# Performance work log

Hardware: AMD Instinct MI355X
Metric: run time of the kernel (lower is better)

Reference implementation:

```python
import jax, jax.numpy as jnp
import numpy as np

B, H, V, MAX_MSG_LEN = 8192, 512, 512, 16


def _uniform(key, shape, scale):
    return jax.random.uniform(key, shape, jnp.float32, -scale, scale)


def setup_inputs() -> dict:
    key = jax.random.key(0)
    ks = jax.random.split(key, 9)
    s = 1.0 / np.sqrt(H)  # torch LSTMCell/Linear default init scale
    return {
        "encoder_hidden": jax.random.normal(ks[0], (B, H), jnp.float32),
        "encoder_cell": jax.random.normal(ks[1], (B, H), jnp.float32),
        "W_ih": _uniform(ks[2], (4 * H, V), s),   # LSTMCell input weights (i,f,g,o)
        "W_hh": _uniform(ks[3], (4 * H, H), s),   # LSTMCell hidden weights
        "b_ih": _uniform(ks[4], (4 * H,), s),
        "b_hh": _uniform(ks[5], (4 * H,), s),
        "W_out": _uniform(ks[6], (V, H), s),      # nn.Linear(hidden, io_size)
        "b_out": _uniform(ks[7], (V,), s),
        "init_input": jnp.zeros((1, V), jnp.float32),  # nn.Parameter zeros
    }


def reference(encoder_hidden, encoder_cell, W_ih, W_hh, b_ih, b_hh, W_out, b_out, init_input):
    batch = encoder_hidden.shape[0]
    x0 = jnp.broadcast_to(init_input, (batch, init_input.shape[1]))

    def step(carry, _):
        x, h, c, m, lp = carry
        # torch LSTMCell: gates ordered (i, f, g, o)
        gates = x @ W_ih.T + b_ih + h @ W_hh.T + b_hh
        i, f, g, o = jnp.split(gates, 4, axis=-1)
        c = jax.nn.sigmoid(f) * c + jax.nn.sigmoid(i) * jnp.tanh(g)
        h = jax.nn.sigmoid(o) * jnp.tanh(c)
        probs = jax.nn.softmax(h @ W_out.T + b_out, axis=1)  # [B, V]
        # eval path: one-hot of argmax
        predict = jax.nn.one_hot(jnp.argmax(probs, axis=1), probs.shape[1], dtype=probs.dtype)
        lp = lp + jnp.log((probs * predict).sum(axis=1)) * m
        new_m = m * (1.0 - predict[:, -1])  # last vocab index acts as EOS
        return (predict, h, c, new_m, lp), (predict, m)

    carry0 = (x0, encoder_hidden, encoder_cell,
              jnp.ones((batch,), jnp.float32), jnp.zeros((batch,), jnp.float32))
    (_, _, _, _, log_probs), (message, masks) = jax.lax.scan(step, carry0, None, length=MAX_MSG_LEN)
    # message: [L, B, V]; mask stacked as [L, 1, B] like torch.stack of [1, B] rows
    return message, masks[:, None, :], log_probs
```

## Files before the change

kernel.cpp:

```cpp
#include <hip/hip_runtime.h>
#include <math.h>

#define Bsz 8192
#define Hd  512
#define Vd  512
#define Ld  16
#define G4  2048
#define NSLAB 16

using short8 = __attribute__((ext_vector_type(8))) short;
using f32x4  = __attribute__((ext_vector_type(4))) float;
using int4v  = __attribute__((ext_vector_type(4))) int;

__device__ __forceinline__ float sigm_f(float x){
  return __builtin_amdgcn_rcpf(1.0f + __expf(-x));
}
__device__ __forceinline__ float tanh_f(float x){
  return 1.0f - 2.0f * __builtin_amdgcn_rcpf(1.0f + __expf(2.0f * x));
}

__device__ __forceinline__ unsigned short f2bf(float f){
  unsigned int u = __float_as_uint(f);
  u = (u + 0x7fffu + ((u >> 16) & 1u)) >> 16;
  return (unsigned short)u;
}
__device__ __forceinline__ float bf2f(unsigned short b){
  return __uint_as_float(((unsigned int)b) << 16);
}

__device__ __forceinline__ void i16split(float x, float S, signed char& a, signed char& b){
  int q = (int)rintf(x * S);
  q = min(max(q, -32640), 32639);
  const int ah = (q + 128) >> 8;
  a = (signed char)ah;
  b = (signed char)(q - (ah << 8));
}

__device__ __forceinline__ void gl_lds16(const void* g, void* l){
  __builtin_amdgcn_global_load_lds((const __attribute__((address_space(1))) void*)g,
                                   (__attribute__((address_space(3))) void*)l, 16, 0, 0);
}

#define C1I (65536.0f / (524288.0f * 32767.0f))
#define C2I (  256.0f / (524288.0f * 32767.0f))

__global__ __launch_bounds__(256) void k_transpose(const float* __restrict__ in,
                                                   float* __restrict__ out){
  __shared__ float tile[32][33];
  const int tx = threadIdx.x, ty = threadIdx.y;
  const int v0 = blockIdx.x * 32, n0 = blockIdx.y * 32;
#pragma unroll
  for(int i=0;i<4;i++)
    tile[ty+i*8][tx] = in[(size_t)(n0+ty+i*8)*Vd + v0+tx];
  __syncthreads();
#pragma unroll
  for(int i=0;i<4;i++)
    out[(size_t)(v0+ty+i*8)*G4 + n0+tx] = tile[tx][ty+i*8];
}

__global__ __launch_bounds__(256) void k_split(const float* __restrict__ src,
                                               unsigned short* __restrict__ hi,
                                               unsigned short* __restrict__ lo, int n){
  const int i = blockIdx.x*256 + threadIdx.x;
  if(i < n){
    const float x = src[i];
    const unsigned short h = f2bf(x);
    hi[i] = h;
    lo[i] = f2bf(x - bf2f(h));
  }
}

__global__ __launch_bounds__(256) void k_split_i8(const float* __restrict__ src,
                                                  signed char* __restrict__ pa,
                                                  signed char* __restrict__ pb,
                                                  float S, int n){
  const int i = blockIdx.x*256 + threadIdx.x;
  if(i < n){
    signed char a, b;
    i16split(src[i], S, a, b);
    pa[i] = a; pb[i] = b;
  }
}

__global__ __launch_bounds__(256, 2) void k_lstm_bf16(
    const unsigned short* __restrict__ hh, const unsigned short* __restrict__ hl,
    const float* __restrict__ cin,
    signed char* __restrict__ ha, signed char* __restrict__ hb,
    float* __restrict__ cout,
    const unsigned short* __restrict__ Whh_hi, const unsigned short* __restrict__ Whh_lo,
    const float* __restrict__ bih, const float* __restrict__ bhh)
{
  __shared__ unsigned short lds[2][16384];
  const int tid = threadIdx.x;
  const int wave = tid >> 6, lane = tid & 63;
  const int mb = blockIdx.x * 128;
  const int jb = blockIdx.y * 32;
  const int b_wave = (wave & 1) * 64;
  const int j_wave = (wave >> 1) * 16;
  const int fr = lane & 15, q = lane >> 4;
  const int lr = lane >> 2, jj = lane & 3;

  auto stage = [&](int k0, int bsel){
    unsigned short* Whi = lds[bsel];
    unsigned short* Wlo = lds[bsel] + 4096;
    unsigned short* Hhi = lds[bsel] + 8192;
    unsigned short* Hlo = lds[bsel] + 12288;
#pragma unroll
    for(int p=0;p<2;p++){
      const int s = wave*2 + p;
      const int r = s*16 + lr;
      const int j = jj ^ ((r >> 1) & 3);
      const size_t ka = (size_t)k0 + j*8;
      const size_t wrow = (size_t)((r >> 5)*Hd + jb + (r & 31));
      gl_lds16(Whh_hi + wrow*Hd + ka, &Whi[s*512]);
      gl_lds16(Whh_lo + wrow*Hd + ka, &Wlo[s*512]);
      gl_lds16(hh + (size_t)(mb + r)*Hd + ka, &Hhi[s*512]);
      gl_lds16(hl + (size_t)(mb + r)*Hd + ka, &Hlo[s*512]);
    }
  };

  stage(0, 0);

  const int j0 = jb + j_wave + q*4;
  float bsum[4][4];
#pragma unroll
  for(int g=0;g<4;g++){
    float4 a = *(const float4*)&bih[g*Hd + j0];
    float4 b = *(const float4*)&bhh[g*Hd + j0];
    bsum[g][0]=a.x+b.x; bsum[g][1]=a.y+b.y; bsum[g][2]=a.z+b.z; bsum[g][3]=a.w+b.w;
  }

  f32x4 acc[4][4];
#pragma unroll
  for(int g=0;g<4;g++)
#pragma unroll
    for(int bt=0;bt<4;bt++) acc[g][bt] = (f32x4){0.f,0.f,0.f,0.f};

  for(int kc=0; kc<16; kc++){
    __syncthreads();
    if(kc < 15) stage((kc+1)*32, (kc+1)&1);

    const unsigned short* Whi = lds[kc&1];
    const unsigned short* Wlo = lds[kc&1] + 4096;
    const unsigned short* Hhi = lds[kc&1] + 8192;
    const unsigned short* Hlo = lds[kc&1] + 12288;

    short8 wh[4], wl[4], hf[4], lf[4];
#pragma unroll
    for(int g=0;g<4;g++){
      const int r = g*32 + j_wave + fr;
      const int off = r*32 + ((q ^ ((r >> 1) & 3)) << 3);
      wh[g] = *(const short8*)&Whi[off];
      wl[g] = *(const short8*)&Wlo[off];
    }
#pragma unroll
    for(int bt=0;bt<4;bt++){
      const int r = b_wave + bt*16 + fr;
      const int off = r*32 + ((q ^ ((r >> 1) & 3)) << 3);
      hf[bt] = *(const short8*)&Hhi[off];
      lf[bt] = *(const short8*)&Hlo[off];
    }
#pragma unroll
    for(int g=0;g<4;g++)
#pragma unroll
      for(int bt=0;bt<4;bt++){
        acc[g][bt] = __builtin_amdgcn_mfma_f32_16x16x32_bf16(wh[g], hf[bt], acc[g][bt], 0,0,0);
        acc[g][bt] = __builtin_amdgcn_mfma_f32_16x16x32_bf16(wh[g], lf[bt], acc[g][bt], 0,0,0);
        acc[g][bt] = __builtin_amdgcn_mfma_f32_16x16x32_bf16(wl[g], hf[bt], acc[g][bt], 0,0,0);
      }
  }

#pragma unroll
  for(int bt=0;bt<4;bt++){
    const int b = mb + b_wave + bt*16 + fr;
    const size_t idx = (size_t)b*Hd + j0;
    float gv[4][4];
#pragma unroll
    for(int g=0;g<4;g++)
#pragma unroll
      for(int r=0;r<4;r++) gv[g][r] = acc[g][bt][r] + bsum[g][r];
    float co[4];
    *(float4*)co = *(const float4*)&cin[idx];
    float cn[4];
    signed char a4[4], b4[4];
#pragma unroll
    for(int r=0;r<4;r++){
      const float I = sigm_f(gv[0][r]);
      const float F = sigm_f(gv[1][r]);
      const float G = tanh_f(gv[2][r]);
      const float O = sigm_f(gv[3][r]);
      cn[r] = F*co[r] + I*G;
      const float hn = O*tanh_f(cn[r]);
      i16split(hn, 32767.0f, a4[r], b4[r]);
    }
    *(float4*)&cout[idx] = *(float4*)cn;
    *(char4*)&ha[idx] = *(char4*)a4;
    *(char4*)&hb[idx] = *(char4*)b4;
  }
}

__global__ __launch_bounds__(256, 2) void k_lstm_i8(
    const signed char* __restrict__ hA, const signed char* __restrict__ hB,
    const float* __restrict__ cin,
    signed char* __restrict__ hoA, signed char* __restrict__ hoB,
    float* __restrict__ cout,
    const signed char* __restrict__ WA, const signed char* __restrict__ WB,
    const float* __restrict__ WihT, const float* __restrict__ bih,
    const float* __restrict__ bhh,
    const float* __restrict__ statM, const float* __restrict__ statS,
    const int* __restrict__ statI,
    float* __restrict__ msg, float* __restrict__ masks_out,
    float* __restrict__ lp_out, float* __restrict__ lpbuf,
    float* __restrict__ mbuf, int prev)
{
  __shared__ unsigned char lds[2][32768];
  __shared__ int gIs[128];
  const int tid = threadIdx.x;
  const int wave = tid >> 6, lane = tid & 63;
  const int mb = blockIdx.x * 128;
  const int jb = blockIdx.y * 32;
  const int b_wave = (wave & 1) * 64;
  const int j_wave = (wave >> 1) * 16;
  const int fr = lane & 15, q = lane >> 4;
  const int lr = lane >> 2, jj = lane & 3;

  auto stage = [&](int k0, int bsel){
    unsigned char* Wa = lds[bsel];
    unsigned char* Wb = lds[bsel] + 8192;
    unsigned char* Ha = lds[bsel] + 16384;
    unsigned char* Hb = lds[bsel] + 24576;
#pragma unroll
    for(int p=0;p<2;p++){
      const int s = wave*2 + p;
      const int r = s*16 + lr;
      const int j = jj ^ ((r >> 1) & 3);
      const size_t ka = (size_t)k0 + j*16;
      const size_t wrow = (size_t)((r >> 5)*Hd + jb + (r & 31));
      gl_lds16(WA + wrow*Hd + ka, &Wa[s*1024]);
      gl_lds16(WB + wrow*Hd + ka, &Wb[s*1024]);
      gl_lds16(hA + (size_t)(mb + r)*Hd + ka, &Ha[s*1024]);
      gl_lds16(hB + (size_t)(mb + r)*Hd + ka, &Hb[s*1024]);
    }
  };

  stage(0, 0);

  if(tid < 128){
    const int row = mb + tid;
    float gm = statM[row]; int gi = statI[row];
#pragma unroll
    for(int s=1;s<NSLAB;s++){
      const float m = statM[(size_t)s*Bsz + row];
      if(m > gm){ gm = m; gi = statI[(size_t)s*Bsz + row]; }
    }
    if(blockIdx.y == 0){
      float tot = 0.0f;
#pragma unroll
      for(int s=0;s<NSLAB;s++)
        tot += statS[(size_t)s*Bsz + row] * __expf(statM[(size_t)s*Bsz + row] - gm);
      const float logp = -__logf(tot);
      const float mo  = (prev == 0) ? 1.0f : mbuf[row];
      const float lpo = (prev == 0) ? 0.0f : lpbuf[row];
      const float lpn = lpo + logp * mo;
      masks_out[(size_t)prev * Bsz + row] = mo;
      lp_out[row] = lpn;
      lpbuf[row]  = lpn;
      mbuf[row]   = mo * ((gi == Vd-1) ? 0.0f : 1.0f);
    }
    gIs[tid] = gi;
  }
  __syncthreads();

  {
    const int r  = tid >> 1;
    const int c0 = jb + (tid & 1) * 16;
    const int gi = gIs[r];
    float* mrow = msg + ((size_t)prev * Bsz + mb + r) * Vd;
#pragma unroll
    for(int i=0;i<4;i++){
      const int c = c0 + i*4;
      float4 v;
      v.x = (c   == gi) ? 1.0f : 0.0f;
      v.y = (c+1 == gi) ? 1.0f : 0.0f;
      v.z = (c+2 == gi) ? 1.0f : 0.0f;
      v.w = (c+3 == gi) ? 1.0f : 0.0f;
      *(float4*)&mrow[c] = v;
    }
  }

  int xid[4];
#pragma unroll
  for(int bt=0;bt<4;bt++)
    xid[bt] = gIs[b_wave + bt*16 + fr];

  int4v acc1[4][4], acc2[4][4];
#pragma unroll
  for(int g=0;g<4;g++)
#pragma unroll
    for(int bt=0;bt<4;bt++){
      acc1[g][bt] = (int4v){0,0,0,0};
      acc2[g][bt] = (int4v){0,0,0,0};
    }

  for(int kc=0; kc<8; kc++){
    __syncthreads();
    if(kc < 7) stage((kc+1)*64, (kc+1)&1);

    const unsigned char* Wa = lds[kc&1];
    const unsigned char* Wb = lds[kc&1] + 8192;
    const unsigned char* Ha = lds[kc&1] + 16384;
    const unsigned char* Hb = lds[kc&1] + 24576;

    int4v wa[4], wb[4], hf[4], lf[4];
#pragma unroll
    for(int g=0;g<4;g++){
      const int r = g*32 + j_wave + fr;
      const int off = r*64 + ((q ^ ((r >> 1) & 3)) << 4);
      wa[g] = *(const int4v*)&Wa[off];
      wb[g] = *(const int4v*)&Wb[off];
    }
#pragma unroll
    for(int bt=0;bt<4;bt++){
      const int r = b_wave + bt*16 + fr;
      const int off = r*64 + ((q ^ ((r >> 1) & 3)) << 4);
      hf[bt] = *(const int4v*)&Ha[off];
      lf[bt] = *(const int4v*)&Hb[off];
    }
#pragma unroll
    for(int g=0;g<4;g++)
#pragma unroll
      for(int bt=0;bt<4;bt++){
        acc1[g][bt] = __builtin_amdgcn_mfma_i32_16x16x64_i8(wa[g], hf[bt], acc1[g][bt], 0,0,0);
        acc2[g][bt] = __builtin_amdgcn_mfma_i32_16x16x64_i8(wa[g], lf[bt], acc2[g][bt], 0,0,0);
        acc2[g][bt] = __builtin_amdgcn_mfma_i32_16x16x64_i8(wb[g], hf[bt], acc2[g][bt], 0,0,0);
      }
  }

  const int j0 = jb + j_wave + q*4;
  float bsum[4][4];
#pragma unroll
  for(int g=0;g<4;g++){
    float4 a = *(const float4*)&bih[g*Hd + j0];
    float4 b = *(const float4*)&bhh[g*Hd + j0];
    bsum[g][0]=a.x+b.x; bsum[g][1]=a.y+b.y; bsum[g][2]=a.z+b.z; bsum[g][3]=a.w+b.w;
  }
#pragma unroll
  for(int bt=0;bt<4;bt++){
    const int b = mb + b_wave + bt*16 + fr;
    const size_t idx = (size_t)b*Hd + j0;
    float gv[4][4];
#pragma unroll
    for(int g=0;g<4;g++)
#pragma unroll
      for(int r=0;r<4;r++)
        gv[g][r] = fmaf(C1I, (float)acc1[g][bt][r],
                   fmaf(C2I, (float)acc2[g][bt][r], bsum[g][r]));
    {
      const float* grow = WihT + (size_t)xid[bt]*G4 + j0;
#pragma unroll
      for(int g=0;g<4;g++){
        float4 x = *(const float4*)&grow[g*Hd];
        gv[g][0]+=x.x; gv[g][1]+=x.y; gv[g][2]+=x.z; gv[g][3]+=x.w;
      }
    }
    float co[4];
    *(float4*)co = *(const float4*)&cin[idx];
    float cn[4];
    signed char a4[4], b4[4];
#pragma unroll
    for(int r=0;r<4;r++){
      const float I = sigm_f(gv[0][r]);
      const float F = sigm_f(gv[1][r]);
      const float G = tanh_f(gv[2][r]);
      const float O = sigm_f(gv[3][r]);
      cn[r] = F*co[r] + I*G;
      const float hn = O*tanh_f(cn[r]);
      i16split(hn, 32767.0f, a4[r], b4[r]);
    }
    *(float4*)&cout[idx] = *(float4*)cn;
    *(char4*)&hoA[idx] = *(char4*)a4;
    *(char4*)&hoB[idx] = *(char4*)b4;
  }
}

__global__ __launch_bounds__(256, 2) void k_logits_i8(
    const signed char* __restrict__ hA, const signed char* __restrict__ hB,
    const signed char* __restrict__ WoA, const signed char* __restrict__ WoB,
    const float* __restrict__ bout,
    float* __restrict__ statM, float* __restrict__ statS, int* __restrict__ statI)
{
  __shared__ unsigned char lds[2][24576];
  const int tid = threadIdx.x;
  const int wave = tid >> 6, lane = tid & 63;
  const int mb = blockIdx.x * 128;
  const int vb = blockIdx.y * 64;
  const int m_wave = (wave & 1) * 64;
  const int n_wave = (wave >> 1) * 32;
  const int fr = lane & 15, q = lane >> 4;
  const int lr = lane >> 2, jj = lane & 3;

  auto stage = [&](int k0, int bsel){
    unsigned char* Ha = lds[bsel];
    unsigned char* Hb = lds[bsel] + 8192;
    unsigned char* Wa = lds[bsel] + 16384;
    unsigned char* Wb = lds[bsel] + 20480;
#pragma unroll
    for(int p=0;p<2;p++){
      const int s = wave*2 + p;
      const int r = s*16 + lr;
      const int j = jj ^ ((r >> 1) & 3);
      const size_t ka = (size_t)k0 + j*16;
      gl_lds16(hA + (size_t)(mb + r)*Hd + ka, &Ha[s*1024]);
      gl_lds16(hB + (size_t)(mb + r)*Hd + ka, &Hb[s*1024]);
    }
    {
      const int r = wave*16 + lr;
      const int j = jj ^ ((r >> 1) & 3);
      const size_t ka = (size_t)k0 + j*16;
      gl_lds16(WoA + (size_t)(vb + r)*Hd + ka, &Wa[wave*1024]);
      gl_lds16(WoB + (size_t)(vb + r)*Hd + ka, &Wb[wave*1024]);
    }
  };

  stage(0, 0);

  int4v acc1[2][4], acc2[2][4];
#pragma unroll
  for(int nt=0;nt<2;nt++)
#pragma unroll
    for(int mt=0;mt<4;mt++){
      acc1[nt][mt] = (int4v){0,0,0,0};
      acc2[nt][mt] = (int4v){0,0,0,0};
    }

  for(int kc=0; kc<8; kc++){
    __syncthreads();
    if(kc < 7) stage((kc+1)*64, (kc+1)&1);

    const unsigned char* Ha = lds[kc&1];
    const unsigned char* Hb = lds[kc&1] + 8192;
    const unsigned char* Wa = lds[kc&1] + 16384;
    const unsigned char* Wb = lds[kc&1] + 20480;

    int4v ah[4], al[4], bh[2], bl[2];
#pragma unroll
    for(int mt=0;mt<4;mt++){
      const int r = m_wave + mt*16 + fr;
      const int off = r*64 + ((q ^ ((r >> 1) & 3)) << 4);
      ah[mt] = *(const int4v*)&Ha[off];
      al[mt] = *(const int4v*)&Hb[off];
    }
#pragma unroll
    for(int nt=0;nt<2;nt++){
      const int r = n_wave + nt*16 + fr;
      const int off = r*64 + ((q ^ ((r >> 1) & 3)) << 4);
      bh[nt] = *(const int4v*)&Wa[off];
      bl[nt] = *(const int4v*)&Wb[off];
    }
#pragma unroll
    for(int nt=0;nt<2;nt++)
#pragma unroll
      for(int mt=0;mt<4;mt++){
        acc1[nt][mt] = __builtin_amdgcn_mfma_i32_16x16x64_i8(ah[mt], bh[nt], acc1[nt][mt], 0,0,0);
        acc2[nt][mt] = __builtin_amdgcn_mfma_i32_16x16x64_i8(ah[mt], bl[nt], acc2[nt][mt], 0,0,0);
        acc2[nt][mt] = __builtin_amdgcn_mfma_i32_16x16x64_i8(al[mt], bh[nt], acc2[nt][mt], 0,0,0);
      }
  }

  const int slab = blockIdx.y*2 + (wave >> 1);
  float bo[2];
  int vv[2];
#pragma unroll
  for(int nt=0;nt<2;nt++){
    vv[nt] = vb + n_wave + nt*16 + fr;
    bo[nt] = bout[vv[nt]];
  }
#pragma unroll
  for(int mt=0;mt<4;mt++){
#pragma unroll
    for(int reg=0;reg<4;reg++){
      float lg[2];
#pragma unroll
      for(int nt=0;nt<2;nt++)
        lg[nt] = fmaf(C1I, (float)acc1[nt][mt][reg],
                 fmaf(C2I, (float)acc2[nt][mt][reg], bo[nt]));
      float vmax = lg[0];
      int   imax = vv[0];
      if(lg[1] > vmax || (lg[1] == vmax && vv[1] < imax)){ vmax = lg[1]; imax = vv[1]; }
#pragma unroll
      for(int off=1; off<16; off<<=1){
        const float vo = __shfl_xor(vmax, off);
        const int   io = __shfl_xor(imax, off);
        if(vo > vmax || (vo == vmax && io < imax)){ vmax = vo; imax = io; }
      }
      float s = __expf(lg[0] - vmax) + __expf(lg[1] - vmax);
#pragma unroll
      for(int off=1; off<16; off<<=1) s += __shfl_xor(s, off);
      if(fr == 0){
        const int m = mb + m_wave + mt*16 + q*4 + reg;
        statM[(size_t)slab*Bsz + m] = vmax;
        statS[(size_t)slab*Bsz + m] = s;
        statI[(size_t)slab*Bsz + m] = imax;
      }
    }
  }
}

__global__ __launch_bounds__(256) void k_merge(
    const float* __restrict__ statM, const float* __restrict__ statS,
    const int* __restrict__ statI,
    float* __restrict__ msg, float* __restrict__ masks_out,
    float* __restrict__ lp_out, float* __restrict__ lpbuf,
    float* __restrict__ mbuf, int step)
{
  __shared__ int gI[32];
  const int tid = threadIdx.x;
  const int mb = blockIdx.x * 32;

  if(tid < 32){
    const int row = mb + tid;
    float gm = statM[row]; int gi = statI[row];
#pragma unroll
    for(int s=1;s<NSLAB;s++){
      const float m = statM[(size_t)s*Bsz + row];
      if(m > gm){ gm = m; gi = statI[(size_t)s*Bsz + row]; }
    }
    float tot = 0.0f;
#pragma unroll
    for(int s=0;s<NSLAB;s++)
      tot += statS[(size_t)s*Bsz + row] * __expf(statM[(size_t)s*Bsz + row] - gm);
    const float logp = -__logf(tot);
    const float mo  = mbuf[row];
    const float lpn = lpbuf[row] + logp * mo;
    masks_out[(size_t)step * Bsz + row] = mo;
    lp_out[row] = lpn;
    gI[tid] = gi;
  }
  __syncthreads();

  const int r  = tid >> 3;
  const int c8 = tid & 7;
  const int gi = gI[r];
  float* mrow = msg + ((size_t)step * Bsz + mb + r) * Vd;
#pragma unroll
  for(int i=0;i<16;i++){
    const int c = (i*8 + c8) * 4;
    float4 v;
    v.x = (c   == gi) ? 1.0f : 0.0f;
    v.y = (c+1 == gi) ? 1.0f : 0.0f;
    v.z = (c+2 == gi) ? 1.0f : 0.0f;
    v.w = (c+3 == gi) ? 1.0f : 0.0f;
    *(float4*)&mrow[c] = v;
  }
}

extern "C" void kernel_launch(void* const* d_in, const int* in_sizes, int n_in,
                              void* d_out, int out_size, void* d_ws, size_t ws_size,
                              hipStream_t stream) {
  const float* enc_h = (const float*)d_in[0];
  const float* enc_c = (const float*)d_in[1];
  const float* Wih   = (const float*)d_in[2];
  const float* Whh   = (const float*)d_in[3];
  const float* bih   = (const float*)d_in[4];
  const float* bhh   = (const float*)d_in[5];
  const float* Wout  = (const float*)d_in[6];
  const float* bout  = (const float*)d_in[7];

  float* out_msg   = (float*)d_out;
  float* out_masks = out_msg + (size_t)Ld * Bsz * Vd;
  float* out_lp    = out_masks + (size_t)Ld * Bsz;

  char* ws = (char*)d_ws;
  float* WihT  = (float*)ws;          ws += (size_t)Vd * G4 * 4;
  unsigned short* WhhHi = (unsigned short*)ws; ws += (size_t)G4 * Hd * 2;
  unsigned short* WhhLo = (unsigned short*)ws; ws += (size_t)G4 * Hd * 2;
  unsigned short* encHi = (unsigned short*)ws; ws += (size_t)Bsz * Hd * 2;
  unsigned short* encLo = (unsigned short*)ws; ws += (size_t)Bsz * Hd * 2;
  signed char* WhhA = (signed char*)ws; ws += (size_t)G4 * Hd;
  signed char* WhhB = (signed char*)ws; ws += (size_t)G4 * Hd;
  signed char* WoA  = (signed char*)ws; ws += (size_t)Vd * Hd;
  signed char* WoB  = (signed char*)ws; ws += (size_t)Vd * Hd;
  signed char* ha0  = (signed char*)ws; ws += (size_t)Bsz * Hd;
  signed char* hb0  = (signed char*)ws; ws += (size_t)Bsz * Hd;
  signed char* ha1  = (signed char*)ws; ws += (size_t)Bsz * Hd;
  signed char* hb1  = (signed char*)ws; ws += (size_t)Bsz * Hd;
  float* cbuf   = (float*)ws;  ws += (size_t)Bsz * Hd * 4;
  float* statM  = (float*)ws;  ws += (size_t)NSLAB * Bsz * 4;
  float* statS  = (float*)ws;  ws += (size_t)NSLAB * Bsz * 4;
  int*   statI  = (int*)ws;    ws += (size_t)NSLAB * Bsz * 4;
  float* lpbuf  = (float*)ws;  ws += (size_t)Bsz * 4;
  float* mbuf   = (float*)ws;  ws += (size_t)Bsz * 4;

  k_transpose<<<dim3(Vd/32, G4/32), dim3(32,8), 0, stream>>>(Wih, WihT);
  k_split<<<(G4*Hd+255)/256, 256, 0, stream>>>(Whh, WhhHi, WhhLo, G4*Hd);
  k_split<<<(Bsz*Hd+255)/256, 256, 0, stream>>>(enc_h, encHi, encLo, Bsz*Hd);
  k_split_i8<<<(G4*Hd+255)/256, 256, 0, stream>>>(Whh, WhhA, WhhB, 524288.0f, G4*Hd);
  k_split_i8<<<(Vd*Hd+255)/256, 256, 0, stream>>>(Wout, WoA, WoB, 524288.0f, Vd*Hd);

  for(int t=0; t<Ld; t++){
    signed char* haOut = (t & 1) ? ha1 : ha0;
    signed char* hbOut = (t & 1) ? hb1 : hb0;
    const signed char* haIn = (t & 1) ? ha0 : ha1;
    const signed char* hbIn = (t & 1) ? hb0 : hb1;

    if(t == 0){
      k_lstm_bf16<<<dim3(Bsz/128, Hd/32), 256, 0, stream>>>(
          encHi, encLo, enc_c, haOut, hbOut, cbuf, WhhHi, WhhLo, bih, bhh);
    } else {
      k_lstm_i8<<<dim3(Bsz/128, Hd/32), 256, 0, stream>>>(
          haIn, hbIn, cbuf, haOut, hbOut, cbuf, WhhA, WhhB, WihT, bih, bhh,
          statM, statS, statI, out_msg, out_masks, out_lp, lpbuf, mbuf, t-1);
    }
    k_logits_i8<<<dim3(Bsz/128, Vd/64), 256, 0, stream>>>(
        haOut, hbOut, WoA, WoB, bout, statM, statS, statI);
  }
  k_merge<<<Bsz/32, 256, 0, stream>>>(statM, statS, statI,
                                      out_msg, out_masks, out_lp,
                                      lpbuf, mbuf, Ld-1);
}
```

Measured before the change: 1.205 ms.

## Load MFMA operands directly from global memory, dropping LDS staging in LSTM and logits kernels

Both int8 MFMA GEMM kernels (LSTM gates and output logits) stop staging W and h tiles through double-buffered LDS with global-to-LDS loads and barriers. Each lane now reads its 16-byte fragments straight from global memory using precomputed row offsets, and the k loop is unrolled by 2. This removes the __syncthreads and LDS traffic and frees LDS for occupancy. In exchange, operands shared across waves are fetched repeatedly through L1/L2, there is no explicit prefetch overlap, and per-lane 16-byte accesses spread across 16 rows are poorly coalesced.

```diff
diff --git a/kernel.cpp b/kernel.cpp
--- a/kernel.cpp
+++ b/kernel.cpp
@@ -213,7 +213,6 @@
     float* __restrict__ lp_out, float* __restrict__ lpbuf,
     float* __restrict__ mbuf, int prev)
 {
-  __shared__ unsigned char lds[2][32768];
   __shared__ int gIs[128];
   const int tid = threadIdx.x;
   const int wave = tid >> 6, lane = tid & 63;
@@ -222,28 +221,6 @@
   const int b_wave = (wave & 1) * 64;
   const int j_wave = (wave >> 1) * 16;
   const int fr = lane & 15, q = lane >> 4;
-  const int lr = lane >> 2, jj = lane & 3;
-
-  auto stage = [&](int k0, int bsel){
-    unsigned char* Wa = lds[bsel];
-    unsigned char* Wb = lds[bsel] + 8192;
-    unsigned char* Ha = lds[bsel] + 16384;
-    unsigned char* Hb = lds[bsel] + 24576;
-#pragma unroll
-    for(int p=0;p<2;p++){
-      const int s = wave*2 + p;
-      const int r = s*16 + lr;
-      const int j = jj ^ ((r >> 1) & 3);
-      const size_t ka = (size_t)k0 + j*16;
-      const size_t wrow = (size_t)((r >> 5)*Hd + jb + (r & 31));
-      gl_lds16(WA + wrow*Hd + ka, &Wa[s*1024]);
-      gl_lds16(WB + wrow*Hd + ka, &Wb[s*1024]);
-      gl_lds16(hA + (size_t)(mb + r)*Hd + ka, &Ha[s*1024]);
-      gl_lds16(hB + (size_t)(mb + r)*Hd + ka, &Hb[s*1024]);
-    }
-  };
-
-  stage(0, 0);
 
   if(tid < 128){
     const int row = mb + tid;
@@ -293,6 +270,14 @@
   for(int bt=0;bt<4;bt++)
     xid[bt] = gIs[b_wave + bt*16 + fr];
 
+  size_t wro[4], hro[4];
+#pragma unroll
+  for(int g=0;g<4;g++)
+    wro[g] = (size_t)(g*Hd + jb + j_wave + fr)*Hd + q*16;
+#pragma unroll
+  for(int bt=0;bt<4;bt++)
+    hro[bt] = (size_t)(mb + b_wave + bt*16 + fr)*Hd + q*16;
+
   int4v acc1[4][4], acc2[4][4];
 #pragma unroll
   for(int g=0;g<4;g++)
@@ -302,29 +287,19 @@
       acc2[g][bt] = (int4v){0,0,0,0};
     }
 
+#pragma unroll 2
   for(int kc=0; kc<8; kc++){
-    __syncthreads();
-    if(kc < 7) stage((kc+1)*64, (kc+1)&1);
-
-    const unsigned char* Wa = lds[kc&1];
-    const unsigned char* Wb = lds[kc&1] + 8192;
-    const unsigned char* Ha = lds[kc&1] + 16384;
-    const unsigned char* Hb = lds[kc&1] + 24576;
-
+    const int kb = kc*64;
     int4v wa[4], wb[4], hf[4], lf[4];
 #pragma unroll
     for(int g=0;g<4;g++){
-      const int r = g*32 + j_wave + fr;
-      const int off = r*64 + ((q ^ ((r >> 1) & 3)) << 4);
-      wa[g] = *(const int4v*)&Wa[off];
-      wb[g] = *(const int4v*)&Wb[off];
+      wa[g] = *(const int4v*)&WA[wro[g] + kb];
+      wb[g] = *(const int4v*)&WB[wro[g] + kb];
     }
 #pragma unroll
     for(int bt=0;bt<4;bt++){
-      const int r = b_wave + bt*16 + fr;
-      const int off = r*64 + ((q ^ ((r >> 1) & 3)) << 4);
-      hf[bt] = *(const int4v*)&Ha[off];
-      lf[bt] = *(const int4v*)&Hb[off];
+      hf[bt] = *(const int4v*)&hA[hro[bt] + kb];
+      lf[bt] = *(const int4v*)&hB[hro[bt] + kb];
     }
 #pragma unroll
     for(int g=0;g<4;g++)
@@ -389,7 +364,6 @@
     const float* __restrict__ bout,
     float* __restrict__ statM, float* __restrict__ statS, int* __restrict__ statI)
 {
-  __shared__ unsigned char lds[2][24576];
   const int tid = threadIdx.x;
   const int wave = tid >> 6, lane = tid & 63;
   const int mb = blockIdx.x * 128;
@@ -397,32 +371,14 @@
   const int m_wave = (wave & 1) * 64;
   const int n_wave = (wave >> 1) * 32;
   const int fr = lane & 15, q = lane >> 4;
-  const int lr = lane >> 2, jj = lane & 3;
-
-  auto stage = [&](int k0, int bsel){
-    unsigned char* Ha = lds[bsel];
-    unsigned char* Hb = lds[bsel] + 8192;
-    unsigned char* Wa = lds[bsel] + 16384;
-    unsigned char* Wb = lds[bsel] + 20480;
-#pragma unroll
-    for(int p=0;p<2;p++){
-      const int s = wave*2 + p;
-      const int r = s*16 + lr;
-      const int j = jj ^ ((r >> 1) & 3);
-      const size_t ka = (size_t)k0 + j*16;
-      gl_lds16(hA + (size_t)(mb + r)*Hd + ka, &Ha[s*1024]);
-      gl_lds16(hB + (size_t)(mb + r)*Hd + ka, &Hb[s*1024]);
-    }
-    {
-      const int r = wave*16 + lr;
-      const int j = jj ^ ((r >> 1) & 3);
-      const size_t ka = (size_t)k0 + j*16;
-      gl_lds16(WoA + (size_t)(vb + r)*Hd + ka, &Wa[wave*1024]);
-      gl_lds16(WoB + (size_t)(vb + r)*Hd + ka, &Wb[wave*1024]);
-    }
-  };
-
-  stage(0, 0);
+
+  size_t mro[4], nro[2];
+#pragma unroll
+  for(int mt=0;mt<4;mt++)
+    mro[mt] = (size_t)(mb + m_wave + mt*16 + fr)*Hd + q*16;
+#pragma unroll
+  for(int nt=0;nt<2;nt++)
+    nro[nt] = (size_t)(vb + n_wave + nt*16 + fr)*Hd + q*16;
 
   int4v acc1[2][4], acc2[2][4];
 #pragma unroll
@@ -433,29 +389,19 @@
       acc2[nt][mt] = (int4v){0,0,0,0};
     }
 
+#pragma unroll 2
   for(int kc=0; kc<8; kc++){
-    __syncthreads();
-    if(kc < 7) stage((kc+1)*64, (kc+1)&1);
-
-    const unsigned char* Ha = lds[kc&1];
-    const unsigned char* Hb = lds[kc&1] + 8192;
-    const unsigned char* Wa = lds[kc&1] + 16384;
-    const unsigned char* Wb = lds[kc&1] + 20480;
-
+    const int kb = kc*64;
     int4v ah[4], al[4], bh[2], bl[2];
 #pragma unroll
     for(int mt=0;mt<4;mt++){
-      const int r = m_wave + mt*16 + fr;
-      const int off = r*64 + ((q ^ ((r >> 1) & 3)) << 4);
-      ah[mt] = *(const int4v*)&Ha[off];
-      al[mt] = *(const int4v*)&Hb[off];
+      ah[mt] = *(const int4v*)&hA[mro[mt] + kb];
+      al[mt] = *(const int4v*)&hB[mro[mt] + kb];
     }
 #pragma unroll
     for(int nt=0;nt<2;nt++){
-      const int r = n_wave + nt*16 + fr;
-      const int off = r*64 + ((q ^ ((r >> 1) & 3)) << 4);
-      bh[nt] = *(const int4v*)&Wa[off];
-      bl[nt] = *(const int4v*)&Wb[off];
+      bh[nt] = *(const int4v*)&WoA[nro[nt] + kb];
+      bl[nt] = *(const int4v*)&WoB[nro[nt] + kb];
     }
 #pragma unroll
     for(int nt=0;nt<2;nt++)
```

Result: slower. 1.968 ms (+63.3%).
